# Optimization experiments

Hardware: AMD Instinct MI355X
Metric: run time of the kernel (lower is better)

Reference implementation:

```python
import jax, jax.numpy as jnp
import numpy as np

KS = 17  # structuring element size
R = KS // 2  # radius 8


def _ellipse_kernel():
    # replicates cv2.getStructuringElement(cv2.MORPH_ELLIPSE, (17, 17)):
    # per row dy, fill columns within dx = round(sqrt(r^2 - dy^2))
    k = np.zeros((KS, KS), np.float32)
    for i in range(KS):
        dy = i - R
        dx = int(round(np.sqrt(max(0.0, float(R * R - dy * dy)))))
        k[i, R - dx:R + dx + 1] = 1.0
    return k


def _morph(v, kern, erode):
    # exact TF min-plus erosion2d / max-plus dilation2d with SAME padding
    # (pad +inf for erosion, -inf for dilation), filters = kern per channel.
    B, H, W, C = v.shape
    pad_val = np.inf if erode else -np.inf
    sgn = -1.0 if erode else 1.0
    red = jnp.min if erode else jnp.max
    comb = jnp.minimum if erode else jnp.maximum
    vp = jnp.pad(v, ((0, 0), (0, 0), (R, R), (0, 0)), constant_values=pad_val)
    X = jnp.stack([vp[:, :, k:k + W, :] for k in range(KS)], axis=0)
    # per kernel row dy: 1D min/max-plus correlation along x
    rows = [red(X + sgn * kern[dy][:, None, None, None, None], axis=0) for dy in range(KS)]
    Rst = jnp.pad(jnp.stack(rows, axis=0), ((0, 0), (0, 0), (R, R), (0, 0), (0, 0)), constant_values=pad_val)
    out = Rst[0][:, 0:H]
    for dy in range(1, KS):
        out = comb(out, Rst[dy][:, dy:dy + H])
    return out


def _mask_edges(masks, kern):
    # flip border rows/cols (corners flipped twice -> original)
    m = jnp.concatenate([1.0 - masks[:, :1], masks[:, 1:-1], 1.0 - masks[:, -1:]], axis=1)
    m = jnp.concatenate([1.0 - m[:, :, :1], m[:, :, 1:-1], 1.0 - m[:, :, -1:]], axis=2)
    eroded = _morph(m, kern, erode=True) + 1.0
    dilated = _morph(m, kern, erode=False) - 1.0
    return dilated - eroded


def setup_inputs() -> dict:
    key = jax.random.key(0)
    k1, k2, k3 = jax.random.split(key, 3)
    B, H, W, C = 8, 512, 512, 3
    in_detections = jax.random.randint(k1, (B, H, W, C), 0, 2).astype(jnp.float32)
    p_detections = jax.random.normal(k2, (B, H, W, C), dtype=jnp.float32)
    edge_weight = 1.0 + 39.0 * jax.random.uniform(k3, (1, 1, 1, C), dtype=jnp.float32)
    in_masks = jnp.ones((B, C), dtype=jnp.float32)
    logvars = -3.0 * jnp.ones((1, C), dtype=jnp.float32)
    return {"in_masks": in_masks, "in_detections": in_detections,
            "p_detections": p_detections, "edge_weight": edge_weight,
            "logvars": logvars}


def reference(in_masks, in_detections, p_detections, edge_weight, logvars):
    kern = jnp.asarray(_ellipse_kernel())
    edges = _mask_edges(in_detections, kern)  # (B,H,W,C)
    weights = 1.0 + (edge_weight - 1.0) * edges
    weights = weights / jnp.sum(weights, axis=(1, 2), keepdims=True)
    pix = jnp.where(in_detections == 1.0,
                    jnp.maximum(0.0, 1.0 - p_detections) ** 2,
                    jnp.maximum(0.0, p_detections) ** 2)
    raw = jnp.sum(weights * pix, axis=(1, 2))  # (B,C)
    losses = jnp.exp(-logvars) * raw + logvars  # (B,C)
    return jnp.mean(in_masks * losses, axis=1)  # (B,)
```

## Files before the change

kernel.cpp:

```cpp
#include <hip/hip_runtime.h>
#include <stdint.h>


#define TILE 16
#define NT   32
#define MAGIC64 0x7F3B9E1DC0FFEE42ull
#define PL(ch, pr) (pl_dyn + ((size_t)((ch) * 32 + (pr))) * 90)

__global__ __launch_bounds__(1024) void k_fused(const float* __restrict__ det,
                                                const float* __restrict__ pdet,
                                                float* partials,
                                                unsigned long long* tags,
                                                const float* __restrict__ in_masks,
                                                const float* __restrict__ ew,
                                                const float* __restrict__ lv,
                                                float* __restrict__ out) {
  extern __shared__ uint64_t pl_dyn[];
  __shared__ uint64_t mb[3][32][9];
  __shared__ uint64_t eg[3][TILE][8];
  __shared__ float red[16][6];
  __shared__ int cw[3][2];
  __shared__ float term[8][3];

  int blk = blockIdx.x;
  int b = blk & 7;
  int tile = blk >> 3;
  int r0 = tile * TILE;
  int tid = threadIdx.x;
  int wv = tid >> 6, lane = tid & 63;

  float dv[8][3];
#pragma unroll
  for (int it = 0; it < 8; ++it) {
    int task = wv * 8 + it;
    int rl = task >> 3, w = task & 7;
    size_t base = (((((size_t)b << 9) + (r0 + rl)) << 9) + (w << 6) + lane) * 3;
    dv[it][0] = det[base];
    dv[it][1] = det[base + 1];
    dv[it][2] = det[base + 2];
  }
#pragma unroll
  for (int it = 0; it < 8; ++it) {
    int task = wv * 8 + it;
    int rl = task >> 3, w = task & 7;
    uint64_t b0 = __ballot(dv[it][0] == 1.0f);
    uint64_t b1 = __ballot(dv[it][1] == 1.0f);
    uint64_t b2 = __ballot(dv[it][2] == 1.0f);
    if (lane == 0) { mb[0][rl + 8][w] = b0; mb[1][rl + 8][w] = b1; mb[2][rl + 8][w] = b2; }
  }
#pragma unroll
  for (int it = 0; it < 8; ++it) {
    int task = wv * 8 + it;
    int rlh = task >> 3, w = task & 7;
    int grow = (rlh < 8) ? (r0 - 8 + rlh) : (r0 + 8 + rlh);
    int mrow = (rlh < 8) ? rlh : (16 + rlh);
    float h0 = 0.f, h1 = 0.f, h2 = 0.f;
    if (grow >= 0 && grow < 512) {
      size_t base = (((((size_t)b << 9) + grow) << 9) + (w << 6) + lane) * 3;
      h0 = det[base]; h1 = det[base + 1]; h2 = det[base + 2];
    }
    uint64_t b0 = __ballot(h0 == 1.0f);
    uint64_t b1 = __ballot(h1 == 1.0f);
    uint64_t b2 = __ballot(h2 == 1.0f);
    if (lane == 0) { mb[0][mrow][w] = b0; mb[1][mrow][w] = b1; mb[2][mrow][w] = b2; }
  }
  __syncthreads();

  float pv[8][3];
#pragma unroll
  for (int it = 0; it < 8; ++it) {
    int task = wv * 8 + it;
    int rl = task >> 3, w = task & 7;
    size_t base = (((((size_t)b << 9) + (r0 + rl)) << 9) + (w << 6) + lane) * 3;
    pv[it][0] = pdet[base];
    pv[it][1] = pdet[base + 1];
    pv[it][2] = pdet[base + 2];
  }

  auto hchain = [&](int ch, int side, int rl, int w) {
    int grow = r0 - 8 + rl;
    bool valid = (grow >= 0 && grow < 512);
    uint64_t x = 0, xl = 0, xh = 0;
    if (valid) {
      x = mb[ch][rl][w];
      xl = (w > 0) ? mb[ch][rl][w - 1] : 0;
      xh = (w < 7) ? mb[ch][rl][w + 1] : 0;
      if (grow == 0 || grow == 511) {
        x = ~x; xl = (w > 0) ? ~xl : 0; xh = (w < 7) ? ~xh : 0;
      }
      if (w == 0) x ^= 1ull;
      if (w == 7) x ^= (1ull << 63);
      if (side) {
        x = ~x; xl = (w > 0) ? ~xl : 0; xh = (w < 7) ? ~xh : 0;
      }
    }
    uint64_t* P = PL(ch, rl);
    if (!side) P[w] = x;
    uint64_t d = x;
#pragma unroll
    for (int s = 1; s <= 8; ++s) {
      d |= (x << s) | (xl >> (64 - s)) | (x >> s) | (xh << (64 - s));
      if (s >= 4) P[(s - 3 + side * 5) * 8 + w] = d;
    }
  };
  {
    hchain(tid >> 9, (tid >> 8) & 1, (tid >> 3) & 31, tid & 7);
    if (tid < 512) hchain(2, tid >> 8, (tid >> 3) & 31, tid & 7);
  }
  __syncthreads();

  const int PD[9] = {5, 5, 5, 4, 4, 3, 2, 1, 0};

  if (tid < 384) {
    int ch = tid >> 7;
    int t3 = tid & 127;
    int rl = t3 >> 3, w = t3 & 7;
    uint64_t dil = 0, erc = 0;
#pragma unroll
    for (int dy = -8; dy <= 8; ++dy) {
      int ady = dy < 0 ? -dy : dy;
      int pr = rl + 8 + dy;
      if (ady == 8) {
        int grow = r0 - 8 + pr;
        uint64_t m = PL(ch, pr)[w];
        dil |= m;
        erc |= (grow >= 0 && grow < 512) ? ~m : 0;
      } else {
        dil |= PL(ch, pr)[PD[ady] * 8 + w];
        erc |= PL(ch, pr)[(PD[ady] + 5) * 8 + w];
      }
    }
    uint64_t e = dil & erc;
    eg[ch][rl][w] = e;
    int c = __popcll(e);
#pragma unroll
    for (int off = 32; off >= 1; off >>= 1) c += __shfl_xor(c, off);
    if (lane == 0) cw[ch][(tid >> 6) & 1] = c;
  }
  __syncthreads();

  float sA0 = 0, sA1 = 0, sA2 = 0, sE0 = 0, sE1 = 0, sE2 = 0;
#pragma unroll
  for (int it = 0; it < 8; ++it) {
    int task = wv * 8 + it;
    int rl = task >> 3, w = task & 7;
    float p0 = pv[it][0], p1 = pv[it][1], p2 = pv[it][2];
    uint64_t E0 = eg[0][rl][w], E1 = eg[1][rl][w], E2 = eg[2][rl][w];
    float v0 = (dv[it][0] == 1.0f) ? 1.0f - p0 : p0; v0 = fmaxf(v0, 0.f); v0 *= v0;
    float v1 = (dv[it][1] == 1.0f) ? 1.0f - p1 : p1; v1 = fmaxf(v1, 0.f); v1 *= v1;
    float v2 = (dv[it][2] == 1.0f) ? 1.0f - p2 : p2; v2 = fmaxf(v2, 0.f); v2 *= v2;
    sA0 += v0; sA1 += v1; sA2 += v2;
    if ((E0 >> lane) & 1) sE0 += v0;
    if ((E1 >> lane) & 1) sE1 += v1;
    if ((E2 >> lane) & 1) sE2 += v2;
  }
#pragma unroll
  for (int off = 32; off >= 1; off >>= 1) {
    sA0 += __shfl_xor(sA0, off); sA1 += __shfl_xor(sA1, off); sA2 += __shfl_xor(sA2, off);
    sE0 += __shfl_xor(sE0, off); sE1 += __shfl_xor(sE1, off); sE2 += __shfl_xor(sE2, off);
  }
  if (lane == 0) {
    red[wv][0] = sA0; red[wv][1] = sA1; red[wv][2] = sA2;
    red[wv][3] = sE0; red[wv][4] = sE1; red[wv][5] = sE2;
  }
  __syncthreads();

  if (tid < 6) {
    float s = 0.f;
    for (int i = 0; i < 16; ++i) s += red[i][tid];
    __hip_atomic_store(&partials[blk * 9 + tid], s,
                       __ATOMIC_RELAXED, __HIP_MEMORY_SCOPE_AGENT);
  } else if (tid < 9) {
    int chx = tid - 6;
    __hip_atomic_store(&partials[blk * 9 + tid], (float)(cw[chx][0] + cw[chx][1]),
                       __ATOMIC_RELAXED, __HIP_MEMORY_SCOPE_AGENT);
  }
  __syncthreads();
  if (tid == 0)
    __hip_atomic_store(&tags[blk], MAGIC64,
                       __ATOMIC_RELEASE, __HIP_MEMORY_SCOPE_AGENT);

  if (blk != 0) return;
  if (tid < 256) {
    while (__hip_atomic_load(&tags[tid], __ATOMIC_ACQUIRE,
                             __HIP_MEMORY_SCOPE_AGENT) != MAGIC64)
      __builtin_amdgcn_s_sleep(8);
  }
  __syncthreads();

  if (tid < 24) {
    int b8 = tid / 3, ch = tid - 3 * b8;
    float sA = 0.f, sE = 0.f, cn = 0.f;
    for (int t = 0; t < NT; ++t) {
      float* P = partials + (size_t)((t << 3) | b8) * 9;
      sA += __hip_atomic_load(&P[ch], __ATOMIC_RELAXED, __HIP_MEMORY_SCOPE_AGENT);
      sE += __hip_atomic_load(&P[3 + ch], __ATOMIC_RELAXED, __HIP_MEMORY_SCOPE_AGENT);
      cn += __hip_atomic_load(&P[6 + ch], __ATOMIC_RELAXED, __HIP_MEMORY_SCOPE_AGENT);
    }
    float w1 = ew[ch] - 1.0f;
    float S = 262144.0f + w1 * cn;
    float raw = (sA + w1 * sE) / S;
    term[b8][ch] = in_masks[b8 * 3 + ch] * (expf(-lv[ch]) * raw + lv[ch]);
  }
  __syncthreads();
  if (tid < 8) out[tid] = (term[tid][0] + term[tid][1] + term[tid][2]) * (1.0f / 3.0f);
}

extern "C" void kernel_launch(void* const* d_in, const int* in_sizes, int n_in,
                              void* d_out, int out_size, void* d_ws, size_t ws_size,
                              hipStream_t stream) {
  const float* in_masks = (const float*)d_in[0];
  const float* det = (const float*)d_in[1];
  const float* pdet = (const float*)d_in[2];
  const float* ew = (const float*)d_in[3];
  const float* lv = (const float*)d_in[4];
  float* out = (float*)d_out;

  float* partials = (float*)d_ws;
  unsigned long long* tags =
      (unsigned long long*)(partials + 256 * 9);

  const int dyn_lds = 3 * 32 * 90 * (int)sizeof(uint64_t);
  (void)hipFuncSetAttribute((const void*)k_fused,
                            hipFuncAttributeMaxDynamicSharedMemorySize, dyn_lds);

  k_fused<<<256, 1024, dyn_lds, stream>>>(det, pdet, partials, tags,
                                          in_masks, ew, lv, out);
}
```

Measured before the change: 20.01 us.

## Move final reduction to a dedicated extra block and prefetch halo rows early

Adds a 257th block that waits on all tile tags and does the final cross-tile reduction with a parallel warp-shuffle reduction, instead of block 0 doing it with a serial 32-iteration loop per thread. Halo row loads are hoisted next to the main tile loads so more global loads are in flight before the ballots. The extra block spins on tags and may occupy a CU while other blocks run, and it depends on co-residency for forward progress.

```diff
diff --git a/kernel.cpp b/kernel.cpp
--- a/kernel.cpp
+++ b/kernel.cpp
@@ -23,11 +23,46 @@
   __shared__ float term[8][3];
 
   int blk = blockIdx.x;
+  int tid = threadIdx.x;
+  int wv = tid >> 6, lane = tid & 63;
+
+  if (blk == 256) {
+    if (tid < 256) {
+      while (__hip_atomic_load(&tags[tid], __ATOMIC_ACQUIRE,
+                               __HIP_MEMORY_SCOPE_AGENT) != MAGIC64)
+        __builtin_amdgcn_s_sleep(8);
+    }
+    __syncthreads();
+    if (tid < 768) {
+      int g = tid >> 5;
+      int b8 = g / 3, ch = g - 3 * b8;
+      int t32 = tid & 31;
+      float* P = partials + (size_t)(((t32) << 3) | b8) * 9;
+      float sA = __hip_atomic_load(&P[ch], __ATOMIC_RELAXED, __HIP_MEMORY_SCOPE_AGENT);
+      float sE = __hip_atomic_load(&P[3 + ch], __ATOMIC_RELAXED, __HIP_MEMORY_SCOPE_AGENT);
+      float cn = __hip_atomic_load(&P[6 + ch], __ATOMIC_RELAXED, __HIP_MEMORY_SCOPE_AGENT);
+#pragma unroll
+      for (int off = 16; off >= 1; off >>= 1) {
+        sA += __shfl_xor(sA, off);
+        sE += __shfl_xor(sE, off);
+        cn += __shfl_xor(cn, off);
+      }
+      if (t32 == 0) {
+        float w1 = ew[ch] - 1.0f;
+        float S = 262144.0f + w1 * cn;
+        float raw = (sA + w1 * sE) / S;
+        term[b8][ch] = in_masks[b8 * 3 + ch] * (expf(-lv[ch]) * raw + lv[ch]);
+      }
+    }
+    __syncthreads();
+    if (tid < 8)
+      out[tid] = (term[tid][0] + term[tid][1] + term[tid][2]) * (1.0f / 3.0f);
+    return;
+  }
+
   int b = blk & 7;
   int tile = blk >> 3;
   int r0 = tile * TILE;
-  int tid = threadIdx.x;
-  int wv = tid >> 6, lane = tid & 63;
 
   float dv[8][3];
 #pragma unroll
@@ -39,6 +74,20 @@
     dv[it][1] = det[base + 1];
     dv[it][2] = det[base + 2];
   }
+  float hv[8][3];
+#pragma unroll
+  for (int it = 0; it < 8; ++it) {
+    int task = wv * 8 + it;
+    int rlh = task >> 3, w = task & 7;
+    int grow = (rlh < 8) ? (r0 - 8 + rlh) : (r0 + 8 + rlh);
+    hv[it][0] = 0.f; hv[it][1] = 0.f; hv[it][2] = 0.f;
+    if (grow >= 0 && grow < 512) {
+      size_t base = (((((size_t)b << 9) + grow) << 9) + (w << 6) + lane) * 3;
+      hv[it][0] = det[base];
+      hv[it][1] = det[base + 1];
+      hv[it][2] = det[base + 2];
+    }
+  }
 #pragma unroll
   for (int it = 0; it < 8; ++it) {
     int task = wv * 8 + it;
@@ -52,16 +101,10 @@
   for (int it = 0; it < 8; ++it) {
     int task = wv * 8 + it;
     int rlh = task >> 3, w = task & 7;
-    int grow = (rlh < 8) ? (r0 - 8 + rlh) : (r0 + 8 + rlh);
     int mrow = (rlh < 8) ? rlh : (16 + rlh);
-    float h0 = 0.f, h1 = 0.f, h2 = 0.f;
-    if (grow >= 0 && grow < 512) {
-      size_t base = (((((size_t)b << 9) + grow) << 9) + (w << 6) + lane) * 3;
-      h0 = det[base]; h1 = det[base + 1]; h2 = det[base + 2];
-    }
-    uint64_t b0 = __ballot(h0 == 1.0f);
-    uint64_t b1 = __ballot(h1 == 1.0f);
-    uint64_t b2 = __ballot(h2 == 1.0f);
+    uint64_t b0 = __ballot(hv[it][0] == 1.0f);
+    uint64_t b1 = __ballot(hv[it][1] == 1.0f);
+    uint64_t b2 = __ballot(hv[it][2] == 1.0f);
     if (lane == 0) { mb[0][mrow][w] = b0; mb[1][mrow][w] = b1; mb[2][mrow][w] = b2; }
   }
   __syncthreads();
@@ -179,31 +222,6 @@
   if (tid == 0)
     __hip_atomic_store(&tags[blk], MAGIC64,
                        __ATOMIC_RELEASE, __HIP_MEMORY_SCOPE_AGENT);
-
-  if (blk != 0) return;
-  if (tid < 256) {
-    while (__hip_atomic_load(&tags[tid], __ATOMIC_ACQUIRE,
-                             __HIP_MEMORY_SCOPE_AGENT) != MAGIC64)
-      __builtin_amdgcn_s_sleep(8);
-  }
-  __syncthreads();
-
-  if (tid < 24) {
-    int b8 = tid / 3, ch = tid - 3 * b8;
-    float sA = 0.f, sE = 0.f, cn = 0.f;
-    for (int t = 0; t < NT; ++t) {
-      float* P = partials + (size_t)((t << 3) | b8) * 9;
-      sA += __hip_atomic_load(&P[ch], __ATOMIC_RELAXED, __HIP_MEMORY_SCOPE_AGENT);
-      sE += __hip_atomic_load(&P[3 + ch], __ATOMIC_RELAXED, __HIP_MEMORY_SCOPE_AGENT);
-      cn += __hip_atomic_load(&P[6 + ch], __ATOMIC_RELAXED, __HIP_MEMORY_SCOPE_AGENT);
-    }
-    float w1 = ew[ch] - 1.0f;
-    float S = 262144.0f + w1 * cn;
-    float raw = (sA + w1 * sE) / S;
-    term[b8][ch] = in_masks[b8 * 3 + ch] * (expf(-lv[ch]) * raw + lv[ch]);
-  }
-  __syncthreads();
-  if (tid < 8) out[tid] = (term[tid][0] + term[tid][1] + term[tid][2]) * (1.0f / 3.0f);
 }
 
 extern "C" void kernel_launch(void* const* d_in, const int* in_sizes, int n_in,
@@ -224,6 +242,6 @@
   (void)hipFuncSetAttribute((const void*)k_fused,
                             hipFuncAttributeMaxDynamicSharedMemorySize, dyn_lds);
 
-  k_fused<<<256, 1024, dyn_lds, stream>>>(det, pdet, partials, tags,
+  k_fused<<<257, 1024, dyn_lds, stream>>>(det, pdet, partials, tags,
                                           in_masks, ew, lv, out);
 }
```

Result: slower. 22.01 us (+10.0%).
